# Performance work log

Hardware: AMD Instinct MI355X
Metric: run time of the kernel (lower is better)

Reference implementation:

```python
import jax, jax.numpy as jnp
import numpy as np

B, T, D, H, FF = 4, 2048, 1024, 16, 4096
HD = D // H
EPS = 1e-5


def setup_inputs() -> dict:
    key = jax.random.key(0)
    ks = jax.random.split(key, 10)
    s = lambda k, shape, fan: jax.random.normal(k, shape, jnp.float32) * (1.0 / np.sqrt(fan))
    return {
        "x": jax.random.normal(ks[0], (B, T, D), jnp.float32),
        "ln1_g": jnp.ones((D,), jnp.float32),
        "ln1_b": jnp.zeros((D,), jnp.float32),
        "qkv_w": s(ks[1], (D, 3 * D), D),
        "qkv_b": jnp.zeros((3 * D,), jnp.float32),
        "proj_w": s(ks[2], (D, D), D),
        "proj_b": jnp.zeros((D,), jnp.float32),
        "ln2_g": jnp.ones((D,), jnp.float32),
        "ln2_b": jnp.zeros((D,), jnp.float32),
        "ff1_w": s(ks[3], (D, FF), D),
        "ff1_b": jnp.zeros((FF,), jnp.float32),
        "ff2_w": s(ks[4], (FF, D), FF),
        "ff2_b": jnp.zeros((D,), jnp.float32),
    }


def _layernorm(x, g, b):
    mu = jnp.mean(x, axis=-1, keepdims=True)
    var = jnp.mean(jnp.square(x - mu), axis=-1, keepdims=True)
    return (x - mu) * jax.lax.rsqrt(var + EPS) * g + b


def reference(x, ln1_g, ln1_b, qkv_w, qkv_b, proj_w, proj_b,
              ln2_g, ln2_b, ff1_w, ff1_b, ff2_w, ff2_b):
    # --- attention sublayer ---
    h = _layernorm(x, ln1_g, ln1_b)
    qkv = h @ qkv_w + qkv_b                      # [B,T,3D]
    q, k, v = jnp.split(qkv, 3, axis=-1)
    q = q.reshape(B, T, H, HD).transpose(0, 2, 1, 3)  # [B,H,T,hd]
    k = k.reshape(B, T, H, HD).transpose(0, 2, 1, 3)
    v = v.reshape(B, T, H, HD).transpose(0, 2, 1, 3)
    att = jnp.einsum('bhqd,bhkd->bhqk', q, k) / np.sqrt(HD)
    causal = jnp.tril(jnp.ones((T, T), bool))
    att = jnp.where(causal, att, jnp.finfo(att.dtype).min)
    att = jax.nn.softmax(att, axis=-1)
    out = jnp.einsum('bhqk,bhkd->bhqd', att, v)  # [B,H,T,hd]
    out = out.transpose(0, 2, 1, 3).reshape(B, T, D)
    x = x + out @ proj_w + proj_b
    # --- MLP sublayer ---
    h = _layernorm(x, ln2_g, ln2_b)
    h = jax.nn.gelu(h @ ff1_w + ff1_b, approximate=True)
    x = x + h @ ff2_w + ff2_b
    return x
```

## Files before the change

kernel.cpp:

```cpp
#include <hip/hip_runtime.h>

typedef __attribute__((ext_vector_type(4))) float f32x4;
typedef __attribute__((ext_vector_type(16))) float f32x16;
typedef __attribute__((ext_vector_type(8))) short s16x8;
typedef __attribute__((ext_vector_type(4))) unsigned short u16x4;
typedef __attribute__((ext_vector_type(4))) unsigned int u32x4;

#define DEV __device__ __forceinline__

DEV unsigned short f2bf(float f) {
  unsigned int u = __float_as_uint(f);
  return (unsigned short)((u + 0x7FFFu + ((u >> 16) & 1u)) >> 16);
}

DEV float exp2_asm(float x) {
  float r; asm("v_exp_f32 %0, %1" : "=v"(r) : "v"(x)); return r;
}
DEV float rcp_asm(float x) {
  float r; asm("v_rcp_f32 %0, %1" : "=v"(r) : "v"(x)); return r;
}
DEV unsigned int pk2(float a, float b) {
  return (__float_as_uint(b) & 0xFFFF0000u) | (__float_as_uint(a) >> 16);
}
DEV void pl32swap(unsigned int& x, unsigned int& y) {
  asm volatile("v_permlane32_swap_b32 %0, %1" : "+v"(x), "+v"(y));
}

DEV void gload_lds16(const void* g, void* l) {
  __builtin_amdgcn_global_load_lds(
      (const __attribute__((address_space(1))) unsigned int*)g,
      (__attribute__((address_space(3))) unsigned int*)l, 16, 0, 0);
}

__global__ __launch_bounds__(256) void ln_kernel(
    const float* __restrict__ x, const float* __restrict__ gam,
    const float* __restrict__ bet, unsigned short* __restrict__ o)
{
  const int row = blockIdx.x;
  const int tid = threadIdx.x;
  f32x4 v = *(const f32x4*)(x + (size_t)row * 1024 + tid * 4);
  float s = v[0] + v[1] + v[2] + v[3];
  float s2 = v[0]*v[0] + v[1]*v[1] + v[2]*v[2] + v[3]*v[3];
  #pragma unroll
  for (int m = 1; m < 64; m <<= 1) { s += __shfl_xor(s, m); s2 += __shfl_xor(s2, m); }
  __shared__ float ps[4], ps2[4];
  const int wid = tid >> 6, lane = tid & 63;
  if (lane == 0) { ps[wid] = s; ps2[wid] = s2; }
  __syncthreads();
  s = ps[0] + ps[1] + ps[2] + ps[3];
  s2 = ps2[0] + ps2[1] + ps2[2] + ps2[3];
  const float mu = s * (1.0f / 1024.0f);
  const float rstd = rsqrtf(s2 * (1.0f / 1024.0f) - mu * mu + 1e-5f);
  f32x4 g4 = *(const f32x4*)(gam + tid * 4);
  f32x4 b4 = *(const f32x4*)(bet + tid * 4);
  u16x4 ov;
  #pragma unroll
  for (int j = 0; j < 4; j++) ov[j] = f2bf((v[j] - mu) * rstd * g4[j] + b4[j]);
  *(u16x4*)(o + (size_t)row * 1024 + tid * 4) = ov;
}

__global__ __launch_bounds__(256) void transpose_kernel(
    const float* __restrict__ W, unsigned short* __restrict__ WT, int K, int N)
{
  __shared__ float tile[64][65];
  const int n0 = blockIdx.x * 64, k0 = blockIdx.y * 64;
  const int c = threadIdx.x & 63, r0 = threadIdx.x >> 6;
  #pragma unroll
  for (int r = r0; r < 64; r += 4)
    tile[r][c] = W[(size_t)(k0 + r) * N + n0 + c];
  __syncthreads();
  #pragma unroll
  for (int r = r0; r < 64; r += 4)
    WT[(size_t)(n0 + r) * K + k0 + c] = f2bf(tile[c][r]);
}

template <int MODE>
__global__ __launch_bounds__(512) void gemm8_kernel(
    const unsigned short* __restrict__ A, const unsigned short* __restrict__ WT,
    const float* __restrict__ bias, const float* resid, void* outp,
    int M, int N, int K)
{
  __shared__ unsigned short lds[3 * 24576];
  const int tid = threadIdx.x;
  const int lane = tid & 63, wid = tid >> 6;
  const int l15 = lane & 15, l4 = lane >> 4;
  const int wm = wid >> 2, wn = wid & 3;
  const int tiles_n = N >> 8;
  const int cpx = gridDim.x >> 3;
  const int id = (blockIdx.x & 7) * cpx + (blockIdx.x >> 3);
  const int bm = id / tiles_n, bn = id % tiles_n;
  const int NT = K >> 6;

  const int srow = tid >> 3;
  const int scol = ((tid & 7) ^ (srow & 7)) * 8;
  const unsigned short* Asrc = A  + (size_t)(bm * 128 + srow) * K + scol;
  const unsigned short* Bsrc = WT + (size_t)(bn * 256 + srow) * K + scol;
  const size_t j64 = (size_t)64 * K;
  const int dwave = wid * 1024;

#define STAGE(t_, ss_) do { \
    char* base_ = (char*)lds + (ss_) * 49152 + dwave; \
    const unsigned short* sA_ = Asrc + (size_t)(t_) * 64; \
    const unsigned short* sB_ = Bsrc + (size_t)(t_) * 64; \
    gload_lds16(sA_,            base_); \
    gload_lds16(sA_ + j64,      base_ + 8192); \
    gload_lds16(sB_,            base_ + 16384); \
    gload_lds16(sB_ + j64,      base_ + 16384 + 8192); \
    gload_lds16(sB_ + 2 * j64,  base_ + 16384 + 16384); \
    gload_lds16(sB_ + 3 * j64,  base_ + 16384 + 24576); \
  } while (0)

  f32x4 acc[4][4] = {};

  const int arow0 = wm * 64 + l15;
  const int brow0 = wn * 64 + l15;
  const int cswz = l15 & 7;

  STAGE(0, 0);
  STAGE(1, 1);
  asm volatile("s_waitcnt vmcnt(6)" ::: "memory");
  __builtin_amdgcn_s_barrier();

  int cs = 0, ss = 2;
  for (int t = 0; t < NT; ++t) {
    const unsigned short* sa = lds + cs * 24576;
    const unsigned short* sb = sa + 8192;
    s16x8 af[4][2], bf[4][2];
    #pragma unroll
    for (int mf = 0; mf < 4; ++mf)
      #pragma unroll
      for (int ks = 0; ks < 2; ++ks)
        af[mf][ks] = *(const s16x8*)&sa[(arow0 + mf * 16) * 64 + (((ks * 4 + l4) ^ cswz) * 8)];
    #pragma unroll
    for (int nf = 0; nf < 4; ++nf)
      #pragma unroll
      for (int ks = 0; ks < 2; ++ks)
        bf[nf][ks] = *(const s16x8*)&sb[(brow0 + nf * 16) * 64 + (((ks * 4 + l4) ^ cswz) * 8)];
    if (t + 2 < NT) STAGE(t + 2, ss);
    __builtin_amdgcn_s_setprio(1);
    #pragma unroll
    for (int mf = 0; mf < 4; ++mf)
      #pragma unroll
      for (int nf = 0; nf < 4; ++nf)
        #pragma unroll
        for (int ks = 0; ks < 2; ++ks)
          acc[mf][nf] = __builtin_amdgcn_mfma_f32_16x16x32_bf16(
              af[mf][ks], bf[nf][ks], acc[mf][nf], 0, 0, 0);
    __builtin_amdgcn_s_setprio(0);
    if (t + 2 < NT)      { asm volatile("s_waitcnt vmcnt(6)" ::: "memory"); }
    else if (t + 1 < NT) { asm volatile("s_waitcnt vmcnt(0)" ::: "memory"); }
    __builtin_amdgcn_s_barrier();
    cs = (cs == 2) ? 0 : cs + 1;
    ss = (ss == 2) ? 0 : ss + 1;
  }
#undef STAGE

  #pragma unroll
  for (int nf = 0; nf < 4; nf++) {
    const int col = bn * 256 + wn * 64 + nf * 16 + l15;
    const float bv = bias[col];
    const float qs = (MODE == 0 && col < 1024) ? 0.18033688f : 1.0f;
    #pragma unroll
    for (int mf = 0; mf < 4; mf++) {
      #pragma unroll
      for (int r = 0; r < 4; r++) {
        const int row = bm * 128 + wm * 64 + mf * 16 + l4 * 4 + r;
        const size_t off = (size_t)row * N + col;
        float v = acc[mf][nf][r] + bv;
        if (MODE == 1) {
          ((float*)outp)[off] = v + resid[off];
        } else if (MODE == 2) {
          const float u = v + 0.044715f * v * v * v;
          const float e = exp2_asm(-2.3022010f * u);
          ((unsigned short*)outp)[off] = f2bf(v * rcp_asm(1.0f + e));
        } else {
          ((unsigned short*)outp)[off] = f2bf(v * qs);
        }
      }
    }
  }
}

__global__ __launch_bounds__(256, 4) void attn_kernel(
    const unsigned short* __restrict__ qkv, unsigned short* __restrict__ outb)
{
  __shared__ unsigned short Ks[2][64 * 64];
  __shared__ unsigned short Vt[64 * 64];
  __shared__ float alf[4][32];
  const int pid = blockIdx.x;
  const int qA = pid, qB = 31 - pid;
  const int bh = blockIdx.y;
  const int b = bh >> 4, h = bh & 15;
  const int tid = threadIdx.x, lane = tid & 63, wid = tid >> 6;
  const int l31 = lane & 31, hi = lane >> 5;
  const int myq = (wid < 2) ? qA : qB;
  const int qbase = myq * 64 + (wid & 1) * 32;
  const size_t base = (size_t)b * 2048 * 3072 + (size_t)h * 64;
  const unsigned short* Qb = qkv + base;
  const unsigned short* Kb = qkv + base + 1024;
  const unsigned short* Vb = qkv + base + 2048;

  s16x8 qf[4];
  {
    const unsigned short* qr = Qb + (size_t)(qbase + l31) * 3072 + hi * 8;
    qf[0] = *(const s16x8*)(qr);
    qf[1] = *(const s16x8*)(qr + 16);
    qf[2] = *(const s16x8*)(qr + 32);
    qf[3] = *(const s16x8*)(qr + 48);
  }

  u16x4 vv[4];
  #pragma unroll
  for (int it = 0; it < 4; ++it) {
    const int cc = tid + 256 * it;
    vv[it] = *(const u16x4*)(Vb + (size_t)(cc >> 4) * 3072 + (cc & 15) * 4);
  }
  #pragma unroll
  for (int s = 0; s < 2; ++s) {
    const int c = s * 256 + tid;
    const int kv = c >> 3;
    const int dsrc = ((c & 7) * 8) ^ ((kv & 7) << 3);
    gload_lds16(Kb + (size_t)kv * 3072 + dsrc, &Ks[0][(size_t)(c & ~63) * 8]);
  }

  f32x16 o0 = {0,0,0,0,0,0,0,0,0,0,0,0,0,0,0,0};
  f32x16 o1 = {0,0,0,0,0,0,0,0,0,0,0,0,0,0,0,0};
  float m = -1e30f, lsum = 0.f;

  for (int kvb = 0; kvb <= qB; ++kvb) {
    const int cur = kvb & 1;
    const int kv0 = kvb * 64;
    __builtin_amdgcn_s_barrier();
    asm volatile("s_waitcnt vmcnt(2)" ::: "memory");
    #pragma unroll
    for (int it = 0; it < 4; ++it) {
      const int cc = tid + 256 * it;
      const int vkv = cc >> 4;
      const int vd = (cc & 15) * 4;
      #pragma unroll
      for (int j = 0; j < 4; j++) {
        const int d = vd + j;
        Vt[d * 64 + (vkv ^ (((d >> 2) & 7) << 3))] = vv[it][j];
      }
    }
    if (kvb < qB) {
      #pragma unroll
      for (int it = 0; it < 4; ++it) {
        const int cc = tid + 256 * it;
        vv[it] = *(const u16x4*)(Vb + (size_t)((kvb + 1) * 64 + (cc >> 4)) * 3072 + (cc & 15) * 4);
      }
      asm volatile("s_waitcnt vmcnt(4)" ::: "memory");
    } else {
      asm volatile("s_waitcnt vmcnt(0)" ::: "memory");
    }
    asm volatile("s_waitcnt lgkmcnt(0)" ::: "memory");
    __builtin_amdgcn_s_barrier();
    if (kvb < qB) {
      #pragma unroll
      for (int s = 0; s < 2; ++s) {
        const int c = s * 256 + tid;
        const int kv = c >> 3;
        const int dsrc = ((c & 7) * 8) ^ ((kv & 7) << 3);
        gload_lds16(Kb + (size_t)((kvb + 1) * 64 + kv) * 3072 + dsrc,
                    &Ks[cur ^ 1][(size_t)(c & ~63) * 8]);
      }
    }

    if (kvb <= myq) {
      const unsigned short* Kc = Ks[cur];
      f32x16 s0 = {0,0,0,0,0,0,0,0,0,0,0,0,0,0,0,0};
      f32x16 s1 = {0,0,0,0,0,0,0,0,0,0,0,0,0,0,0,0};
      __builtin_amdgcn_s_setprio(1);
      #pragma unroll
      for (int c = 0; c < 4; ++c) {
        const int koff = ((2 * c + hi) ^ (l31 & 7)) * 8;
        s16x8 k0 = *(const s16x8*)&Kc[l31 * 64 + koff];
        s16x8 k1 = *(const s16x8*)&Kc[(32 + l31) * 64 + koff];
        s0 = __builtin_amdgcn_mfma_f32_32x32x16_bf16(k0, qf[c], s0, 0, 0, 0);
        s1 = __builtin_amdgcn_mfma_f32_32x32x16_bf16(k1, qf[c], s1, 0, 0, 0);
      }
      __builtin_amdgcn_s_setprio(0);
      if (kv0 + 63 > qbase) {
        const int thr = qbase + l31 - kv0;
        #pragma unroll
        for (int r = 0; r < 16; ++r) {
          const int kvl = (r & 3) + 8 * (r >> 2) + 4 * hi;
          if (kvl > thr)      s0[r] = -3.0e38f;
          if (kvl + 32 > thr) s1[r] = -3.0e38f;
        }
      }
      float mx = s0[0];
      #pragma unroll
      for (int r = 1; r < 16; ++r) mx = fmaxf(mx, s0[r]);
      #pragma unroll
      for (int r = 0; r < 16; ++r) mx = fmaxf(mx, s1[r]);
      mx = fmaxf(mx, __shfl_xor(mx, 32));
      const bool skip = __all(mx <= m + 11.5f);
      const float mnew = skip ? m : fmaxf(m, mx);
      float rsum = 0.f;
      #pragma unroll
      for (int r = 0; r < 16; ++r) { s0[r] = exp2_asm(s0[r] - mnew); rsum += s0[r]; }
      #pragma unroll
      for (int r = 0; r < 16; ++r) { s1[r] = exp2_asm(s1[r] - mnew); rsum += s1[r]; }
      rsum += __shfl_xor(rsum, 32);
      if (skip) {
        lsum += rsum;
      } else {
        const float alpha = exp2_asm(m - mnew);
        lsum = lsum * alpha + rsum;
        m = mnew;
        alf[wid][l31] = alpha;
        #pragma unroll
        for (int r = 0; r < 16; ++r) {
          const float ar = alf[wid][(r & 3) + 8 * (r >> 2) + 4 * hi];
          o0[r] *= ar; o1[r] *= ar;
        }
      }
      s16x8 pa[4];
      #pragma unroll
      for (int kb = 0; kb < 2; ++kb) {
        #pragma unroll
        for (int cc = 0; cc < 2; ++cc) {
          const int rb = cc * 8;
          unsigned int X0, Y0, X1, Y1;
          if (kb == 0) {
            X0 = pk2(s0[rb + 0], s0[rb + 1]); Y0 = pk2(s0[rb + 4], s0[rb + 5]);
            X1 = pk2(s0[rb + 2], s0[rb + 3]); Y1 = pk2(s0[rb + 6], s0[rb + 7]);
          } else {
            X0 = pk2(s1[rb + 0], s1[rb + 1]); Y0 = pk2(s1[rb + 4], s1[rb + 5]);
            X1 = pk2(s1[rb + 2], s1[rb + 3]); Y1 = pk2(s1[rb + 6], s1[rb + 7]);
          }
          pl32swap(X0, Y0);
          pl32swap(X1, Y1);
          u32x4 w = {X0, X1, Y0, Y1};
          pa[kb * 2 + cc] = __builtin_bit_cast(s16x8, w);
        }
      }
      const int voff = l31 >> 2;
      __builtin_amdgcn_s_setprio(1);
      #pragma unroll
      for (int c = 0; c < 4; ++c) {
        const int off = ((2 * c + hi) ^ voff) * 8;
        s16x8 v0 = *(const s16x8*)&Vt[l31 * 64 + off];
        s16x8 v1 = *(const s16x8*)&Vt[(32 + l31) * 64 + off];
        o0 = __builtin_amdgcn_mfma_f32_32x32x16_bf16(pa[c], v0, o0, 0, 0, 0);
        o1 = __builtin_amdgcn_mfma_f32_32x32x16_bf16(pa[c], v1, o1, 0, 0, 0);
      }
      __builtin_amdgcn_s_setprio(0);
    }
  }

  const float iv = rcp_asm(lsum);
  alf[wid][l31] = iv;
  unsigned short* ob = outb + ((size_t)b * 2048 + qbase) * 1024 + h * 64 + l31;
  #pragma unroll
  for (int r = 0; r < 16; ++r) {
    const int ql = (r & 3) + 8 * (r >> 2) + 4 * hi;
    const float ir = alf[wid][ql];
    ob[(size_t)ql * 1024]      = f2bf(o0[r] * ir);
    ob[(size_t)ql * 1024 + 32] = f2bf(o1[r] * ir);
  }
}

extern "C" void kernel_launch(void* const* d_in, const int* in_sizes, int n_in,
                              void* d_out, int out_size, void* d_ws, size_t ws_size,
                              hipStream_t stream) {
  const float* x      = (const float*)d_in[0];
  const float* ln1_g  = (const float*)d_in[1];
  const float* ln1_b  = (const float*)d_in[2];
  const float* qkv_w  = (const float*)d_in[3];
  const float* qkv_b  = (const float*)d_in[4];
  const float* proj_w = (const float*)d_in[5];
  const float* proj_b = (const float*)d_in[6];
  const float* ln2_g  = (const float*)d_in[7];
  const float* ln2_b  = (const float*)d_in[8];
  const float* ff1_w  = (const float*)d_in[9];
  const float* ff1_b  = (const float*)d_in[10];
  const float* ff2_w  = (const float*)d_in[11];
  const float* ff2_b  = (const float*)d_in[12];
  float* out = (float*)d_out;

  char* ws = (char*)d_ws;
  size_t off = 0;
  unsigned short* wbuf   = (unsigned short*)(ws + off); off += (size_t)4096 * 1024 * 2;
  unsigned short* hbuf   = (unsigned short*)(ws + off); off += (size_t)8192 * 1024 * 2;
  unsigned short* qkvbuf = (unsigned short*)(ws + off); off += (size_t)8192 * 3072 * 2;
  unsigned short* gbuf   = (unsigned short*)(ws + off);

  ln_kernel<<<8192, 256, 0, stream>>>(x, ln1_g, ln1_b, hbuf);
  transpose_kernel<<<dim3(3072 / 64, 1024 / 64), 256, 0, stream>>>(qkv_w, wbuf, 1024, 3072);
  gemm8_kernel<0><<<dim3(64 * 12), 512, 0, stream>>>(hbuf, wbuf, qkv_b, nullptr, qkvbuf,
                                                     8192, 3072, 1024);
  attn_kernel<<<dim3(16, 64), 256, 0, stream>>>(qkvbuf, hbuf);
  transpose_kernel<<<dim3(1024 / 64, 1024 / 64), 256, 0, stream>>>(proj_w, wbuf, 1024, 1024);
  gemm8_kernel<1><<<dim3(64 * 4), 512, 0, stream>>>(hbuf, wbuf, proj_b, x, out,
                                                    8192, 1024, 1024);
  ln_kernel<<<8192, 256, 0, stream>>>(out, ln2_g, ln2_b, hbuf);
  transpose_kernel<<<dim3(4096 / 64, 1024 / 64), 256, 0, stream>>>(ff1_w, wbuf, 1024, 4096);
  gemm8_kernel<2><<<dim3(64 * 16), 512, 0, stream>>>(hbuf, wbuf, ff1_b, nullptr, gbuf,
                                                     8192, 4096, 1024);
  transpose_kernel<<<dim3(1024 / 64, 4096 / 64), 256, 0, stream>>>(ff2_w, wbuf, 4096, 1024);
  gemm8_kernel<1><<<dim3(64 * 4), 512, 0, stream>>>(gbuf, wbuf, ff2_b, out, out,
                                                    8192, 1024, 4096);
}
```

Baseline: 455.5 us.

## Split GEMM k-loop into four barrier-synced phases interleaving LDS reads, prefetch and MFMA

Restructures the GEMM main loop into four phases per K tile. Each phase loads a subset of A/B fragments from LDS, issues part of the next-tile global-to-LDS prefetch, synchronises all waves with a barrier plus an lgkmcnt wait, then runs eight MFMAs. The goal is to cut register pressure, since only 6 fragments are live instead of 16, and to keep waves in lockstep so memory and matrix work interleave the way hipBLASLt-style ping-pong kernels do. In exchange it adds four workgroup barriers per iteration, which can stall waves, and fragment reuse is lower within each phase.

Result: slower. 465.5 us (+2.2%).

```diff
diff --git a/kernel.cpp b/kernel.cpp
--- a/kernel.cpp
+++ b/kernel.cpp
@@ -98,16 +98,23 @@
   const size_t j64 = (size_t)64 * K;
   const int dwave = wid * 1024;
 
-#define STAGE(t_, ss_) do { \
+#define STAGE_A(t_, ss_) do { \
     char* base_ = (char*)lds + (ss_) * 49152 + dwave; \
     const unsigned short* sA_ = Asrc + (size_t)(t_) * 64; \
+    gload_lds16(sA_,       base_); \
+    gload_lds16(sA_ + j64, base_ + 8192); \
+  } while (0)
+#define STAGE_B0(t_, ss_) do { \
+    char* base_ = (char*)lds + (ss_) * 49152 + dwave + 16384; \
     const unsigned short* sB_ = Bsrc + (size_t)(t_) * 64; \
-    gload_lds16(sA_,            base_); \
-    gload_lds16(sA_ + j64,      base_ + 8192); \
-    gload_lds16(sB_,            base_ + 16384); \
-    gload_lds16(sB_ + j64,      base_ + 16384 + 8192); \
-    gload_lds16(sB_ + 2 * j64,  base_ + 16384 + 16384); \
-    gload_lds16(sB_ + 3 * j64,  base_ + 16384 + 24576); \
+    gload_lds16(sB_,       base_); \
+    gload_lds16(sB_ + j64, base_ + 8192); \
+  } while (0)
+#define STAGE_B1(t_, ss_) do { \
+    char* base_ = (char*)lds + (ss_) * 49152 + dwave + 16384 + 16384; \
+    const unsigned short* sB_ = Bsrc + 2 * j64 + (size_t)(t_) * 64; \
+    gload_lds16(sB_,       base_); \
+    gload_lds16(sB_ + j64, base_ + 8192); \
   } while (0)
 
   f32x4 acc[4][4] = {};
@@ -116,8 +123,14 @@
   const int brow0 = wn * 64 + l15;
   const int cswz = l15 & 7;
 
-  STAGE(0, 0);
-  STAGE(1, 1);
+#define RDA(mf_, ks_) (*(const s16x8*)&sa[(arow0 + (mf_) * 16) * 64 + ((((ks_) * 4 + l4) ^ cswz) * 8)])
+#define RDB(nf_, ks_) (*(const s16x8*)&sb[(brow0 + (nf_) * 16) * 64 + ((((ks_) * 4 + l4) ^ cswz) * 8)])
+#define PH_SYNC  __builtin_amdgcn_s_barrier(); \
+                 asm volatile("s_waitcnt lgkmcnt(0)" ::: "memory"); \
+                 __builtin_amdgcn_sched_barrier(0)
+
+  STAGE_A(0, 0); STAGE_B0(0, 0); STAGE_B1(0, 0);
+  STAGE_A(1, 1); STAGE_B0(1, 1); STAGE_B1(1, 1);
   asm volatile("s_waitcnt vmcnt(6)" ::: "memory");
   __builtin_amdgcn_s_barrier();
 
@@ -125,35 +138,64 @@
   for (int t = 0; t < NT; ++t) {
     const unsigned short* sa = lds + cs * 24576;
     const unsigned short* sb = sa + 8192;
-    s16x8 af[4][2], bf[4][2];
-    #pragma unroll
-    for (int mf = 0; mf < 4; ++mf)
-      #pragma unroll
-      for (int ks = 0; ks < 2; ++ks)
-        af[mf][ks] = *(const s16x8*)&sa[(arow0 + mf * 16) * 64 + (((ks * 4 + l4) ^ cswz) * 8)];
-    #pragma unroll
-    for (int nf = 0; nf < 4; ++nf)
-      #pragma unroll
-      for (int ks = 0; ks < 2; ++ks)
-        bf[nf][ks] = *(const s16x8*)&sb[(brow0 + nf * 16) * 64 + (((ks * 4 + l4) ^ cswz) * 8)];
-    if (t + 2 < NT) STAGE(t + 2, ss);
+    const bool pf = (t + 2 < NT);
+    s16x8 afx[2], bfx[4];
+    afx[0] = RDA(0, 0); afx[1] = RDA(1, 0);
+    bfx[0] = RDB(0, 0); bfx[1] = RDB(1, 0); bfx[2] = RDB(2, 0); bfx[3] = RDB(3, 0);
+    if (pf) STAGE_A(t + 2, ss);
+    PH_SYNC;
     __builtin_amdgcn_s_setprio(1);
     #pragma unroll
-    for (int mf = 0; mf < 4; ++mf)
-      #pragma unroll
-      for (int nf = 0; nf < 4; ++nf)
-        #pragma unroll
-        for (int ks = 0; ks < 2; ++ks)
-          acc[mf][nf] = __builtin_amdgcn_mfma_f32_16x16x32_bf16(
-              af[mf][ks], bf[nf][ks], acc[mf][nf], 0, 0, 0);
+    for (int nf = 0; nf < 4; ++nf) {
+      acc[0][nf] = __builtin_amdgcn_mfma_f32_16x16x32_bf16(afx[0], bfx[nf], acc[0][nf], 0, 0, 0);
+      acc[1][nf] = __builtin_amdgcn_mfma_f32_16x16x32_bf16(afx[1], bfx[nf], acc[1][nf], 0, 0, 0);
+    }
     __builtin_amdgcn_s_setprio(0);
-    if (t + 2 < NT)      { asm volatile("s_waitcnt vmcnt(6)" ::: "memory"); }
-    else if (t + 1 < NT) { asm volatile("s_waitcnt vmcnt(0)" ::: "memory"); }
+    __builtin_amdgcn_s_barrier();
+    afx[0] = RDA(2, 0); afx[1] = RDA(3, 0);
+    if (pf) STAGE_B0(t + 2, ss);
+    PH_SYNC;
+    __builtin_amdgcn_s_setprio(1);
+    #pragma unroll
+    for (int nf = 0; nf < 4; ++nf) {
+      acc[2][nf] = __builtin_amdgcn_mfma_f32_16x16x32_bf16(afx[0], bfx[nf], acc[2][nf], 0, 0, 0);
+      acc[3][nf] = __builtin_amdgcn_mfma_f32_16x16x32_bf16(afx[1], bfx[nf], acc[3][nf], 0, 0, 0);
+    }
+    __builtin_amdgcn_s_setprio(0);
+    __builtin_amdgcn_s_barrier();
+    afx[0] = RDA(0, 1); afx[1] = RDA(1, 1);
+    bfx[0] = RDB(0, 1); bfx[1] = RDB(1, 1); bfx[2] = RDB(2, 1); bfx[3] = RDB(3, 1);
+    if (pf) STAGE_B1(t + 2, ss);
+    PH_SYNC;
+    __builtin_amdgcn_s_setprio(1);
+    #pragma unroll
+    for (int nf = 0; nf < 4; ++nf) {
+      acc[0][nf] = __builtin_amdgcn_mfma_f32_16x16x32_bf16(afx[0], bfx[nf], acc[0][nf], 0, 0, 0);
+      acc[1][nf] = __builtin_amdgcn_mfma_f32_16x16x32_bf16(afx[1], bfx[nf], acc[1][nf], 0, 0, 0);
+    }
+    __builtin_amdgcn_s_setprio(0);
+    __builtin_amdgcn_s_barrier();
+    afx[0] = RDA(2, 1); afx[1] = RDA(3, 1);
+    PH_SYNC;
+    __builtin_amdgcn_s_setprio(1);
+    #pragma unroll
+    for (int nf = 0; nf < 4; ++nf) {
+      acc[2][nf] = __builtin_amdgcn_mfma_f32_16x16x32_bf16(afx[0], bfx[nf], acc[2][nf], 0, 0, 0);
+      acc[3][nf] = __builtin_amdgcn_mfma_f32_16x16x32_bf16(afx[1], bfx[nf], acc[3][nf], 0, 0, 0);
+    }
+    __builtin_amdgcn_s_setprio(0);
+    if (pf)                { asm volatile("s_waitcnt vmcnt(6)" ::: "memory"); }
+    else if (t + 1 < NT)   { asm volatile("s_waitcnt vmcnt(0)" ::: "memory"); }
     __builtin_amdgcn_s_barrier();
     cs = (cs == 2) ? 0 : cs + 1;
     ss = (ss == 2) ? 0 : ss + 1;
   }
-#undef STAGE
+#undef STAGE_A
+#undef STAGE_B0
+#undef STAGE_B1
+#undef RDA
+#undef RDB
+#undef PH_SYNC
 
   #pragma unroll
   for (int nf = 0; nf < 4; nf++) {
```
